# Kernel tuning notes

Measured on AMD Instinct MI355X. Metric: run time of the kernel, lower is better.

The kernel has to match this reference:

```python
import jax, jax.numpy as jnp
import numpy as np

DIM = 320
HEADS = 8
GROUPS = 32
KV_DIM = 768


def group_norm(x, scale, bias, groups=GROUPS, eps=1e-6):
    b, c, h, w = x.shape
    xg = x.reshape(b, groups, c // groups, h, w)
    mu = xg.mean(axis=(2, 3, 4), keepdims=True)
    var = xg.var(axis=(2, 3, 4), keepdims=True)
    xg = (xg - mu) * jax.lax.rsqrt(var + eps)
    x = xg.reshape(b, c, h, w)
    return x * scale[None, :, None, None] + bias[None, :, None, None]


def layer_norm(x, scale, bias, eps=1e-5):
    mu = x.mean(-1, keepdims=True)
    var = x.var(-1, keepdims=True)
    return (x - mu) * jax.lax.rsqrt(var + eps) * scale + bias


def cross_attention(x, kv, wq, wk, wv, wo, bo, heads=HEADS):
    # weights stored as [in, out] (transposed vs torch Linear)
    b, lq, d = x.shape
    lk = kv.shape[1]
    dh = d // heads
    q = (x @ wq).reshape(b, lq, heads, dh).transpose(0, 2, 1, 3)
    k = (kv @ wk).reshape(b, lk, heads, dh).transpose(0, 2, 1, 3)
    v = (kv @ wv).reshape(b, lk, heads, dh).transpose(0, 2, 1, 3)
    scores = jnp.einsum('bhqd,bhkd->bhqk', q, k) * (dh ** -0.5)
    attn = jax.nn.softmax(scores, axis=-1)
    out = jnp.einsum('bhqk,bhkd->bhqd', attn, v)
    out = out.transpose(0, 2, 1, 3).reshape(b, lq, d)
    return out @ wo + bo


def setup_inputs() -> dict:
    key = jax.random.key(0)
    ks = jax.random.split(key, 24)
    d = DIM
    s = 0.02
    inp = {
        'q': jax.random.normal(ks[0], (2, d, 64, 64), jnp.float32),
        'kv': jax.random.normal(ks[1], (2, 77, KV_DIM), jnp.float32),
        'gn_s': jnp.ones((d,), jnp.float32),
        'gn_b': jnp.zeros((d,), jnp.float32),
        'cin_w': jax.random.normal(ks[2], (d, d), jnp.float32) * s,
        'cin_b': jnp.zeros((d,), jnp.float32),
        'ln0_s': jnp.ones((d,), jnp.float32),
        'ln0_b': jnp.zeros((d,), jnp.float32),
        'a1_wq': jax.random.normal(ks[3], (d, d), jnp.float32) * s,
        'a1_wk': jax.random.normal(ks[4], (d, d), jnp.float32) * s,
        'a1_wv': jax.random.normal(ks[5], (d, d), jnp.float32) * s,
        'a1_wo': jax.random.normal(ks[6], (d, d), jnp.float32) * s,
        'a1_bo': jnp.zeros((d,), jnp.float32),
        'ln1_s': jnp.ones((d,), jnp.float32),
        'ln1_b': jnp.zeros((d,), jnp.float32),
        'a2_wq': jax.random.normal(ks[7], (d, d), jnp.float32) * s,
        'a2_wk': jax.random.normal(ks[8], (KV_DIM, d), jnp.float32) * s,
        'a2_wv': jax.random.normal(ks[9], (KV_DIM, d), jnp.float32) * s,
        'a2_wo': jax.random.normal(ks[10], (d, d), jnp.float32) * s,
        'a2_bo': jnp.zeros((d,), jnp.float32),
        'lnA_s': jnp.ones((d,), jnp.float32),
        'lnA_b': jnp.zeros((d,), jnp.float32),
        'fc0_w': jax.random.normal(ks[11], (d, 8 * d), jnp.float32) * s,
        'fc0_b': jnp.zeros((8 * d,), jnp.float32),
        'fc1_w': jax.random.normal(ks[12], (4 * d, d), jnp.float32) * s,
        'fc1_b': jnp.zeros((d,), jnp.float32),
        'cout_w': jax.random.normal(ks[13], (d, d), jnp.float32) * s,
        'cout_b': jnp.zeros((d,), jnp.float32),
    }
    return inp


def reference(q, kv, gn_s, gn_b, cin_w, cin_b, ln0_s, ln0_b,
              a1_wq, a1_wk, a1_wv, a1_wo, a1_bo, ln1_s, ln1_b,
              a2_wq, a2_wk, a2_wv, a2_wo, a2_bo, lnA_s, lnA_b,
              fc0_w, fc0_b, fc1_w, fc1_b, cout_w, cout_b):
    b, c, h, w = q.shape
    res1 = q
    x = group_norm(q, gn_s, gn_b)
    # 1x1 conv == channel matmul
    x = jnp.einsum('bchw,co->bohw', x, cin_w) + cin_b[None, :, None, None]
    x = x.transpose(0, 2, 3, 1).reshape(b, h * w, c)
    xn = layer_norm(x, ln0_s, ln0_b)
    x = cross_attention(xn, xn, a1_wq, a1_wk, a1_wv, a1_wo, a1_bo) + x
    x = cross_attention(layer_norm(x, ln1_s, ln1_b), kv,
                        a2_wq, a2_wk, a2_wv, a2_wo, a2_bo) + x
    res2 = x
    g = layer_norm(x, lnA_s, lnA_b) @ fc0_w + fc0_b
    half = g.shape[-1] // 2
    # GEGLU: value * GELU(gate); torch nn.GELU default is exact (erf)
    g = g[..., :half] * jax.nn.gelu(g[..., half:], approximate=False)
    x = g @ fc1_w + fc1_b + res2
    x = x.reshape(b, h, w, c).transpose(0, 3, 1, 2)
    x = jnp.einsum('bchw,co->bohw', x, cout_w) + cout_b[None, :, None, None] + res1
    return x
```

## Files before the change

### kernel.cpp

```cpp
#include <hip/hip_runtime.h>
#include <math.h>

typedef short short8 __attribute__((ext_vector_type(8)));
typedef float floatx4 __attribute__((ext_vector_type(4)));
typedef unsigned short ushort_t;
typedef unsigned int uint_t;

constexpr int BATCH   = 2;
constexpr int DIM     = 320;
constexpr int NHEADS  = 8;
constexpr int DH      = 40;
constexpr int NGROUPS = 32;
constexpr int CPG     = 10;
constexpr int SPATIAL = 4096;
constexpr int ROWS    = BATCH * SPATIAL;
constexpr int KVL     = 77;
constexpr int KVD     = 768;
constexpr int FF      = 1280;
constexpr int TQ      = 128;

#define QK_EXP2_SCALE 0.2281259062f

__device__ __forceinline__ ushort_t f2bf(float f) {
    uint_t u = __float_as_uint(f);
    u += 0x7FFFu + ((u >> 16) & 1u);
    return (ushort_t)(u >> 16);
}

__device__ __forceinline__ void gld16(const ushort_t* g, ushort_t* l) {
    __builtin_amdgcn_global_load_lds(
        (const __attribute__((address_space(1))) void*)g,
        (__attribute__((address_space(3))) void*)l, 16, 0, 0);
}

__global__ void zero_stats_kernel(float* stats) {
    if (threadIdx.x < 128) stats[threadIdx.x] = 0.f;
}

__global__ __launch_bounds__(256) void gn_partial_kernel(const float* __restrict__ q,
                                                         float* __restrict__ stats) {
    int slice = blockIdx.x, bg = blockIdx.y;
    const float* base = q + (size_t)bg * (CPG * SPATIAL) + slice * 2560;
    float s = 0.f, ss = 0.f;
#pragma unroll
    for (int j = 0; j < 10; j++) {
        float v = base[j * 256 + threadIdx.x];
        s += v; ss += v * v;
    }
    __shared__ float rs[256], rss[256];
    rs[threadIdx.x] = s; rss[threadIdx.x] = ss;
    __syncthreads();
    for (int off = 128; off > 0; off >>= 1) {
        if (threadIdx.x < off) {
            rs[threadIdx.x]  += rs[threadIdx.x + off];
            rss[threadIdx.x] += rss[threadIdx.x + off];
        }
        __syncthreads();
    }
    if (threadIdx.x == 0) {
        atomicAdd(&stats[bg * 2],     rs[0]);
        atomicAdd(&stats[bg * 2 + 1], rss[0]);
    }
}

__global__ void gn_apply_transpose_kernel(const float* __restrict__ q,
                                          const float* __restrict__ stats,
                                          const float* __restrict__ gs,
                                          const float* __restrict__ gb,
                                          ushort_t* __restrict__ out) {
    __shared__ float tile[32][33];
    int l0 = blockIdx.x * 32, c0 = blockIdx.y * 32, b = blockIdx.z;
    int tx = threadIdx.x, ty = threadIdx.y;
    int c = c0 + ty;
    int g = c / CPG;
    float s  = stats[(b * NGROUPS + g) * 2];
    float ss = stats[(b * NGROUPS + g) * 2 + 1];
    const float invn = 1.f / 40960.f;
    float mean = s * invn;
    float rstd = rsqrtf(ss * invn - mean * mean + 1e-6f);
    float v = q[((size_t)(b * DIM + c)) * SPATIAL + l0 + tx];
    tile[ty][tx] = (v - mean) * rstd * gs[c] + gb[c];
    __syncthreads();
    out[((size_t)(b * SPATIAL + l0 + ty)) * DIM + c0 + tx] = f2bf(tile[tx][ty]);
}

__global__ void out_transpose_kernel(const float* __restrict__ xin,
                                     const float* __restrict__ q,
                                     float* __restrict__ out) {
    __shared__ float tile[32][33];
    int l0 = blockIdx.x * 32, c0 = blockIdx.y * 32, b = blockIdx.z;
    int tx = threadIdx.x, ty = threadIdx.y;
    tile[ty][tx] = xin[((size_t)(b * SPATIAL + l0 + ty)) * DIM + c0 + tx];
    __syncthreads();
    size_t oi = ((size_t)(b * DIM + c0 + ty)) * SPATIAL + l0 + tx;
    out[oi] = tile[tx][ty] + q[oi];
}

__global__ __launch_bounds__(64) void ln_kernel(const float* __restrict__ x,
                                                const float* __restrict__ sc,
                                                const float* __restrict__ bi,
                                                ushort_t* __restrict__ out) {
    int row = blockIdx.x;
    const float* xr = x + (size_t)row * DIM;
    float v[5];
    float sum = 0.f, sq = 0.f;
#pragma unroll
    for (int j = 0; j < 5; j++) {
        v[j] = xr[threadIdx.x + j * 64];
        sum += v[j]; sq += v[j] * v[j];
    }
#pragma unroll
    for (int off = 32; off > 0; off >>= 1) {
        sum += __shfl_down(sum, off);
        sq  += __shfl_down(sq, off);
    }
    sum = __shfl(sum, 0); sq = __shfl(sq, 0);
    float mean = sum / (float)DIM;
    float rstd = rsqrtf(sq / (float)DIM - mean * mean + 1e-5f);
#pragma unroll
    for (int j = 0; j < 5; j++) {
        int i = threadIdx.x + j * 64;
        out[(size_t)row * DIM + i] = f2bf((v[j] - mean) * rstd * sc[i] + bi[i]);
    }
}

struct WSeg { const float* src; ushort_t* dst; int K; int N; int t0; };
struct WTab { WSeg s[12]; };

__global__ __launch_bounds__(256) void wtrans_all_kernel(WTab tab) {
    __shared__ float tile[32][33];
    int bid = blockIdx.x;
    int si = 0;
#pragma unroll
    for (int i = 1; i < 12; i++) if (bid >= tab.s[i].t0) si = i;
    WSeg sg = tab.s[si];
    int local = bid - sg.t0;
    int ntn = sg.N >> 5;
    int kt = local / ntn, nt = local - kt * ntn;
    int n0 = nt * 32, k0 = kt * 32;
    int tx = threadIdx.x & 31, ty8 = threadIdx.x >> 5;
    for (int r = ty8; r < 32; r += 8)
        tile[r][tx] = sg.src[(size_t)(k0 + r) * sg.N + n0 + tx];
    __syncthreads();
    for (int r = ty8; r < 32; r += 8)
        sg.dst[(size_t)(n0 + r) * sg.K + k0 + tx] = f2bf(tile[tx][r]);
}

__global__ void cvt_bf16_kernel(const float* __restrict__ src, ushort_t* __restrict__ dst, int n) {
    int i = blockIdx.x * 256 + threadIdx.x;
    if (i < n) dst[i] = f2bf(src[i]);
}

__global__ __launch_bounds__(256) void gemm128_kernel(
    const ushort_t* __restrict__ A, const ushort_t* __restrict__ Wt,
    const float* __restrict__ bias, const float* __restrict__ resid,
    float* __restrict__ Cf, ushort_t* __restrict__ Cb,
    int M, int N, int K, float qsc, int ncut)
{
    __shared__ __align__(16) ushort_t As[128][64];
    __shared__ __align__(16) ushort_t Bs[64][64];
    int tid = threadIdx.x;
    int wave = tid >> 6, lane = tid & 63;
    int l15 = tid & 15, quad = lane >> 4;
    int m0 = blockIdx.x * 128, n0 = blockIdx.y * 64;
    int lrow = lane >> 3, slot = lane & 7;
    floatx4 acc[2][4] = {};

    for (int k0 = 0; k0 < K; k0 += 64) {
#pragma unroll
        for (int t = 0; t < 4; t++) {
            int task = wave * 4 + t;
            int r = task * 8 + lrow;
            int gc = slot ^ (r & 7);
            gld16(&A[(size_t)(m0 + r) * K + k0 + gc * 8], &As[task * 8][0]);
        }
#pragma unroll
        for (int t = 0; t < 2; t++) {
            int task = wave * 2 + t;
            int r = task * 8 + lrow;
            int gc = slot ^ (r & 7);
            gld16(&Wt[(size_t)(n0 + r) * K + k0 + gc * 8], &Bs[task * 8][0]);
        }
        __syncthreads();
        short8 a[2][2], b[4][2];
#pragma unroll
        for (int g = 0; g < 2; g++) {
            int r = 32 * wave + 16 * g + l15;
            a[g][0] = *(const short8*)&As[r][(quad ^ (r & 7)) * 8];
            a[g][1] = *(const short8*)&As[r][((4 + quad) ^ (r & 7)) * 8];
        }
#pragma unroll
        for (int t = 0; t < 4; t++) {
            int r = 16 * t + l15;
            b[t][0] = *(const short8*)&Bs[r][(quad ^ (r & 7)) * 8];
            b[t][1] = *(const short8*)&Bs[r][((4 + quad) ^ (r & 7)) * 8];
        }
#pragma unroll
        for (int g = 0; g < 2; g++)
#pragma unroll
            for (int t = 0; t < 4; t++) {
                acc[g][t] = __builtin_amdgcn_mfma_f32_16x16x32_bf16(a[g][0], b[t][0], acc[g][t], 0, 0, 0);
                acc[g][t] = __builtin_amdgcn_mfma_f32_16x16x32_bf16(a[g][1], b[t][1], acc[g][t], 0, 0, 0);
            }
        __syncthreads();
    }

#pragma unroll
    for (int g = 0; g < 2; g++) {
        int mrow = m0 + 32 * wave + 16 * g + quad * 4;
#pragma unroll
        for (int t = 0; t < 4; t++) {
            int n = n0 + 16 * t + l15;
            float bv = bias ? bias[n] : 0.f;
            float sc = (n < ncut) ? qsc : 1.f;
#pragma unroll
            for (int i = 0; i < 4; i++) {
                int m = mrow + i;
                float v = acc[g][t][i] + bv;
                if (resid) v += resid[(size_t)m * N + n];
                v *= sc;
                if (Cf) Cf[(size_t)m * N + n] = v;
                if (Cb) Cb[(size_t)m * N + n] = f2bf(v);
            }
        }
    }
}

__global__ __launch_bounds__(256) void geglu128_kernel(
    const ushort_t* __restrict__ A, const ushort_t* __restrict__ Wt,
    const float* __restrict__ bias, ushort_t* __restrict__ C, int M)
{
    constexpr int K = 320;
    __shared__ __align__(16) ushort_t As[128][64];
    __shared__ __align__(16) ushort_t Bv[64][64];
    __shared__ __align__(16) ushort_t Bg[64][64];
    int tid = threadIdx.x;
    int wave = tid >> 6, lane = tid & 63;
    int l15 = tid & 15, quad = lane >> 4;
    int m0 = blockIdx.x * 128, n0 = blockIdx.y * 64;
    int lrow = lane >> 3, slot = lane & 7;
    floatx4 av[2][4] = {}, ag[2][4] = {};

    for (int k0 = 0; k0 < K; k0 += 64) {
#pragma unroll
        for (int t = 0; t < 4; t++) {
            int task = wave * 4 + t;
            int r = task * 8 + lrow;
            int gc = slot ^ (r & 7);
            gld16(&A[(size_t)(m0 + r) * K + k0 + gc * 8], &As[task * 8][0]);
        }
#pragma unroll
        for (int t = 0; t < 2; t++) {
            int task = wave * 2 + t;
            int r = task * 8 + lrow;
            int gc = slot ^ (r & 7);
            gld16(&Wt[(size_t)(n0 + r) * K + k0 + gc * 8],        &Bv[task * 8][0]);
            gld16(&Wt[(size_t)(FF + n0 + r) * K + k0 + gc * 8],   &Bg[task * 8][0]);
        }
        __syncthreads();
        short8 a[2][2], bv[4][2], bg[4][2];
#pragma unroll
        for (int g = 0; g < 2; g++) {
            int r = 32 * wave + 16 * g + l15;
            a[g][0] = *(const short8*)&As[r][(quad ^ (r & 7)) * 8];
            a[g][1] = *(const short8*)&As[r][((4 + quad) ^ (r & 7)) * 8];
        }
#pragma unroll
        for (int t = 0; t < 4; t++) {
            int r = 16 * t + l15;
            bv[t][0] = *(const short8*)&Bv[r][(quad ^ (r & 7)) * 8];
            bv[t][1] = *(const short8*)&Bv[r][((4 + quad) ^ (r & 7)) * 8];
            bg[t][0] = *(const short8*)&Bg[r][(quad ^ (r & 7)) * 8];
            bg[t][1] = *(const short8*)&Bg[r][((4 + quad) ^ (r & 7)) * 8];
        }
#pragma unroll
        for (int g = 0; g < 2; g++)
#pragma unroll
            for (int t = 0; t < 4; t++) {
                av[g][t] = __builtin_amdgcn_mfma_f32_16x16x32_bf16(a[g][0], bv[t][0], av[g][t], 0, 0, 0);
                av[g][t] = __builtin_amdgcn_mfma_f32_16x16x32_bf16(a[g][1], bv[t][1], av[g][t], 0, 0, 0);
                ag[g][t] = __builtin_amdgcn_mfma_f32_16x16x32_bf16(a[g][0], bg[t][0], ag[g][t], 0, 0, 0);
                ag[g][t] = __builtin_amdgcn_mfma_f32_16x16x32_bf16(a[g][1], bg[t][1], ag[g][t], 0, 0, 0);
            }
        __syncthreads();
    }

#pragma unroll
    for (int g = 0; g < 2; g++) {
        int mrow = m0 + 32 * wave + 16 * g + quad * 4;
#pragma unroll
        for (int t = 0; t < 4; t++) {
            int n = n0 + 16 * t + l15;
            float bb = bias[n], bgte = bias[FF + n];
#pragma unroll
            for (int i = 0; i < 4; i++) {
                float val  = av[g][t][i] + bb;
                float gate = ag[g][t][i] + bgte;
                float gl = 0.5f * gate * (1.f + erff(gate * 0.70710678118654752f));
                C[(size_t)(mrow + i) * FF + n] = f2bf(val * gl);
            }
        }
    }
}

__global__ __launch_bounds__(256) void gemm_small_kernel(
    const ushort_t* __restrict__ A, const ushort_t* __restrict__ Wt,
    ushort_t* __restrict__ Cb, int M, int N, int K)
{
    __shared__ __align__(16) ushort_t As[64][72];
    __shared__ __align__(16) ushort_t Bs[64][72];
    int tid = threadIdx.x;
    int wave = tid >> 6, l15 = tid & 15, quad = (tid & 63) >> 4;
    int m0 = blockIdx.x * 64, n0 = blockIdx.y * 64;
    floatx4 acc[4] = {};

    for (int k0 = 0; k0 < K; k0 += 64) {
#pragma unroll
        for (int p = 0; p < 2; p++) {
            int lin = p * 256 + tid;
            int r = lin >> 3, c8 = (lin & 7) * 8;
            int m = m0 + r;
            short8 avv = {};
            if (m < M) avv = *(const short8*)&A[(size_t)m * K + k0 + c8];
            *(short8*)&As[r][c8] = avv;
            *(short8*)&Bs[r][c8] = *(const short8*)&Wt[(size_t)(n0 + r) * K + k0 + c8];
        }
        __syncthreads();
        short8 a0 = *(const short8*)&As[16 * wave + l15][quad * 8];
        short8 a1 = *(const short8*)&As[16 * wave + l15][32 + quad * 8];
#pragma unroll
        for (int t = 0; t < 4; t++) {
            short8 b0 = *(const short8*)&Bs[16 * t + l15][quad * 8];
            short8 b1 = *(const short8*)&Bs[16 * t + l15][32 + quad * 8];
            acc[t] = __builtin_amdgcn_mfma_f32_16x16x32_bf16(a0, b0, acc[t], 0, 0, 0);
            acc[t] = __builtin_amdgcn_mfma_f32_16x16x32_bf16(a1, b1, acc[t], 0, 0, 0);
        }
        __syncthreads();
    }
    int mrow = m0 + 16 * wave + quad * 4;
#pragma unroll
    for (int t = 0; t < 4; t++) {
        int n = n0 + 16 * t + l15;
#pragma unroll
        for (int i = 0; i < 4; i++) {
            int m = mrow + i;
            if (m < M) Cb[(size_t)m * N + n] = f2bf(acc[t][i]);
        }
    }
}

template <int NPARTS>
__global__ __launch_bounds__(256) void flash_kernel(
    const ushort_t* __restrict__ Qg, const ushort_t* __restrict__ Kg,
    const ushort_t* __restrict__ Vg, ushort_t* __restrict__ Og,
    float* __restrict__ Opart, float* __restrict__ Lpart,
    int sQ, int sKV, int nk)
{
    __shared__ __align__(16) ushort_t QPs[8][130][8];
    __shared__ __align__(16) ushort_t Ks[8][64][8];
    __shared__ __align__(16) ushort_t VsT[48][72];

    int tid = threadIdx.x;
    int wave = tid >> 6, lane = tid & 63;
    int l15 = tid & 15, quad = lane >> 4;
    int qt = blockIdx.x, h = blockIdx.y;
    int b, kp;
    if (NPARTS == 2) { b = blockIdx.z >> 1; kp = blockIdx.z & 1; }
    else             { b = blockIdx.z;      kp = 0; }
    int q0 = qt * TQ;

    const ushort_t* Qb = Qg + (size_t)(b * SPATIAL + q0) * sQ + h * DH;
    const ushort_t* Kb = Kg + (size_t)b * nk * sKV + h * DH;
    const ushort_t* Vb = Vg + (size_t)b * nk * sKV + h * DH;

    const short8 z8 = {};
    for (int i = tid; i < 3 * 64; i += 256)
        *(short8*)&Ks[5 + (i >> 6)][i & 63][0] = z8;
    for (int i = tid; i < 8 * 72; i += 256)
        VsT[40 + i / 72][i % 72] = 0;
    if (tid < 72) VsT[40][tid] = 0x3F80;

    for (int t5 = wave; t5 < 10; t5 += 4) {
        int cid = t5 >> 1, half = t5 & 1;
        gld16(&Qb[(size_t)(half * 64 + lane) * sQ + cid * 8], &QPs[cid][half * 64][0]);
    }
    __syncthreads();

    short8 aq[2][2];
#pragma unroll
    for (int g = 0; g < 2; g++) {
        int r = 32 * wave + 16 * g + l15;
        aq[g][0] = *(const short8*)&QPs[quad][r][0];
        aq[g][1] = *(const short8*)&QPs[4 + quad][r][0];
    }

    floatx4 o[2][3] = {};

    int ntiles_all = (nk + 63) >> 6;
    int t_lo = (NPARTS == 2) ? kp * (ntiles_all >> 1) : 0;
    int t_hi = (NPARTS == 2) ? t_lo + (ntiles_all >> 1) : ntiles_all;

    for (int t = t_lo; t < t_hi; t++) {
        int k0 = t * 64;
        __syncthreads();
        for (int c = wave; c < 5; c += 4)
            gld16(&Kb[(size_t)(k0 + lane) * sKV + c * 8], &Ks[c][0][0]);
        for (int tk = tid; tk < 320; tk += 256) {
            int row = tk & 63, cid = tk >> 6;
            int kr = k0 + row;
            short8 v8 = z8;
            if (kr < nk) v8 = *(const short8*)&Vb[(size_t)kr * sKV + cid * 8];
#pragma unroll
            for (int j = 0; j < 8; j++) VsT[cid * 8 + j][row] = v8[j];
        }
        __syncthreads();

        floatx4 s[2][4] = {};
#pragma unroll
        for (int tt = 0; tt < 4; tt++) {
            short8 b0 = *(const short8*)&Ks[quad][16 * tt + l15][0];
            short8 b1 = *(const short8*)&Ks[4 + quad][16 * tt + l15][0];
#pragma unroll
            for (int g = 0; g < 2; g++) {
                s[g][tt] = __builtin_amdgcn_mfma_f32_16x16x32_bf16(aq[g][0], b0, s[g][tt], 0, 0, 0);
                s[g][tt] = __builtin_amdgcn_mfma_f32_16x16x32_bf16(aq[g][1], b1, s[g][tt], 0, 0, 0);
            }
        }

        bool full = (k0 + 64 <= nk);
#pragma unroll
        for (int g = 0; g < 2; g++) {
#pragma unroll
            for (int i = 0; i < 4; i++) {
                int row = 32 * wave + 16 * g + 4 * quad + i;
#pragma unroll
                for (int tt = 0; tt < 4; tt++) {
                    float x = s[g][tt][i];
                    if (!full && (k0 + 16 * tt + l15 >= nk)) x = -1e30f;
                    float pf = exp2f(x);
                    QPs[2 * tt + (l15 >> 3)][row][l15 & 7] =
                        (ushort_t)(__float_as_uint(pf) >> 16);
                }
            }
        }

        short8 vb[3][2];
#pragma unroll
        for (int t2 = 0; t2 < 3; t2++) {
            vb[t2][0] = *(const short8*)&VsT[16 * t2 + l15][quad * 8];
            vb[t2][1] = *(const short8*)&VsT[16 * t2 + l15][32 + quad * 8];
        }
#pragma unroll
        for (int g = 0; g < 2; g++) {
            int r = 32 * wave + 16 * g + l15;
            short8 p0 = *(const short8*)&QPs[quad][r][0];
            short8 p1 = *(const short8*)&QPs[4 + quad][r][0];
#pragma unroll
            for (int t2 = 0; t2 < 3; t2++) {
                o[g][t2] = __builtin_amdgcn_mfma_f32_16x16x32_bf16(p0, vb[t2][0], o[g][t2], 0, 0, 0);
                o[g][t2] = __builtin_amdgcn_mfma_f32_16x16x32_bf16(p1, vb[t2][1], o[g][t2], 0, 0, 0);
            }
        }
    }

    if (NPARTS == 1) {
        float inv[2][4];
#pragma unroll
        for (int g = 0; g < 2; g++)
#pragma unroll
            for (int i = 0; i < 4; i++)
                inv[g][i] = 1.f / __shfl(o[g][2][i], (lane & 48) | 8, 64);
#pragma unroll
        for (int g = 0; g < 2; g++)
#pragma unroll
            for (int t2 = 0; t2 < 3; t2++) {
                int c = 16 * t2 + l15;
                if (c < DH) {
#pragma unroll
                    for (int i = 0; i < 4; i++) {
                        size_t row = (size_t)(b * SPATIAL + q0 + 32 * wave + 16 * g + 4 * quad + i);
                        Og[row * DIM + h * DH + c] = f2bf(o[g][t2][i] * inv[g][i]);
                    }
                }
            }
    } else {
#pragma unroll
        for (int g = 0; g < 2; g++) {
#pragma unroll
            for (int t2 = 0; t2 < 3; t2++) {
                int c = 16 * t2 + l15;
                if (c < DH) {
#pragma unroll
                    for (int i = 0; i < 4; i++) {
                        size_t row = (size_t)(b * SPATIAL + q0 + 32 * wave + 16 * g + 4 * quad + i);
                        Opart[((size_t)kp * ROWS + row) * DIM + h * DH + c] = o[g][t2][i];
                    }
                }
            }
            if (l15 == 8) {
#pragma unroll
                for (int i = 0; i < 4; i++) {
                    size_t row = (size_t)(b * SPATIAL + q0 + 32 * wave + 16 * g + 4 * quad + i);
                    Lpart[((size_t)kp * ROWS + row) * NHEADS + h] = o[g][2][i];
                }
            }
        }
    }
}

__global__ __launch_bounds__(320) void attn_merge_kernel(
    const float* __restrict__ Op, const float* __restrict__ Lp,
    ushort_t* __restrict__ Og)
{
    int row = blockIdx.x, c = threadIdx.x;
    int h = c / DH;
    float l = Lp[(size_t)row * NHEADS + h] + Lp[((size_t)ROWS + row) * NHEADS + h];
    float o = Op[(size_t)row * DIM + c] + Op[((size_t)ROWS + row) * DIM + c];
    Og[(size_t)row * DIM + c] = f2bf(o / l);
}

extern "C" void kernel_launch(void* const* d_in, const int* in_sizes, int n_in,
                              void* d_out, int out_size, void* d_ws, size_t ws_size,
                              hipStream_t stream) {
    (void)in_sizes; (void)n_in; (void)out_size; (void)ws_size;
    const float* q      = (const float*)d_in[0];
    const float* kv     = (const float*)d_in[1];
    const float* gn_s   = (const float*)d_in[2];
    const float* gn_b   = (const float*)d_in[3];
    const float* cin_w  = (const float*)d_in[4];
    const float* cin_b  = (const float*)d_in[5];
    const float* ln0_s  = (const float*)d_in[6];
    const float* ln0_b  = (const float*)d_in[7];
    const float* a1_wq  = (const float*)d_in[8];
    const float* a1_wk  = (const float*)d_in[9];
    const float* a1_wv  = (const float*)d_in[10];
    const float* a1_wo  = (const float*)d_in[11];
    const float* a1_bo  = (const float*)d_in[12];
    const float* ln1_s  = (const float*)d_in[13];
    const float* ln1_b  = (const float*)d_in[14];
    const float* a2_wq  = (const float*)d_in[15];
    const float* a2_wk  = (const float*)d_in[16];
    const float* a2_wv  = (const float*)d_in[17];
    const float* a2_wo  = (const float*)d_in[18];
    const float* a2_bo  = (const float*)d_in[19];
    const float* lnA_s  = (const float*)d_in[20];
    const float* lnA_b  = (const float*)d_in[21];
    const float* fc0_w  = (const float*)d_in[22];
    const float* fc0_b  = (const float*)d_in[23];
    const float* fc1_w  = (const float*)d_in[24];
    const float* fc1_b  = (const float*)d_in[25];
    const float* cout_w = (const float*)d_in[26];
    const float* cout_b = (const float*)d_in[27];
    float* out = (float*)d_out;

    char* p = (char*)d_ws;
    auto carve = [&](size_t bytes) -> char* {
        char* r = p;
        p += (bytes + 255) & ~(size_t)255;
        return r;
    };
    float*    stats  = (float*)carve(512);
    float*    B0     = (float*)carve((size_t)ROWS * DIM * 4);
    float*    B2     = (float*)carve((size_t)ROWS * DIM * 4);
    ushort_t* gnO    = (ushort_t*)carve((size_t)ROWS * DIM * 2);
    ushort_t* ln0O   = (ushort_t*)carve((size_t)ROWS * DIM * 2);
    ushort_t* QKV    = (ushort_t*)carve((size_t)ROWS * 960 * 2);
    ushort_t* attnO  = (ushort_t*)carve((size_t)ROWS * DIM * 2);
    ushort_t* ln1O   = (ushort_t*)carve((size_t)ROWS * DIM * 2);
    ushort_t* Q2     = (ushort_t*)carve((size_t)ROWS * DIM * 2);
    ushort_t* KVc    = (ushort_t*)carve((size_t)BATCH * KVL * 640 * 2);
    ushort_t* lnAO   = (ushort_t*)carve((size_t)ROWS * DIM * 2);
    ushort_t* GLU    = (ushort_t*)carve((size_t)ROWS * FF * 2);
    ushort_t* X2     = (ushort_t*)carve((size_t)ROWS * DIM * 2);
    ushort_t* kvbf   = (ushort_t*)carve((size_t)BATCH * KVL * KVD * 2);
    ushort_t* qkv_t  = (ushort_t*)carve((size_t)960 * 320 * 2);
    ushort_t* cin_t  = (ushort_t*)carve((size_t)320 * 320 * 2);
    ushort_t* a1wo_t = (ushort_t*)carve((size_t)320 * 320 * 2);
    ushort_t* a2wq_t = (ushort_t*)carve((size_t)320 * 320 * 2);
    ushort_t* kvx_t  = (ushort_t*)carve((size_t)640 * 768 * 2);
    ushort_t* a2wo_t = (ushort_t*)carve((size_t)320 * 320 * 2);
    ushort_t* fc0_t  = (ushort_t*)carve((size_t)2560 * 320 * 2);
    ushort_t* fc1_t  = (ushort_t*)carve((size_t)320 * 1280 * 2);
    ushort_t* cout_t = (ushort_t*)carve((size_t)320 * 320 * 2);
    float* Opart = (float*)GLU;
    float* Lpart = (float*)gnO;

    auto gemm = [&](const ushort_t* A, const ushort_t* Wt, const float* bias,
                    const float* resid, float* Cf, ushort_t* Cb,
                    int M, int N, int K, float qsc = 1.f, int ncut = 0) {
        gemm128_kernel<<<dim3(M / 128, N / 64), 256, 0, stream>>>(
            A, Wt, bias, resid, Cf, Cb, M, N, K, qsc, ncut);
    };

    {
        WTab tab;
        int t0 = 0;
        auto seg = [&](int i, const float* s, ushort_t* d, int K, int N) {
            tab.s[i] = {s, d, K, N, t0};
            t0 += (K / 32) * (N / 32);
        };
        seg(0,  cin_w,  cin_t,             320, 320);
        seg(1,  a1_wq,  qkv_t,             320, 320);
        seg(2,  a1_wk,  qkv_t + 320 * 320, 320, 320);
        seg(3,  a1_wv,  qkv_t + 640 * 320, 320, 320);
        seg(4,  a1_wo,  a1wo_t,            320, 320);
        seg(5,  a2_wq,  a2wq_t,            320, 320);
        seg(6,  a2_wk,  kvx_t,             768, 320);
        seg(7,  a2_wv,  kvx_t + 320 * 768, 768, 320);
        seg(8,  a2_wo,  a2wo_t,            320, 320);
        seg(9,  fc0_w,  fc0_t,             320, 2560);
        seg(10, fc1_w,  fc1_t,             1280, 320);
        seg(11, cout_w, cout_t,            320, 320);
        wtrans_all_kernel<<<t0, 256, 0, stream>>>(tab);
    }
    {
        int n = BATCH * KVL * KVD;
        cvt_bf16_kernel<<<(n + 255) / 256, 256, 0, stream>>>(kv, kvbf, n);
    }

    zero_stats_kernel<<<1, 128, 0, stream>>>(stats);
    gn_partial_kernel<<<dim3(16, 64), 256, 0, stream>>>(q, stats);
    gn_apply_transpose_kernel<<<dim3(SPATIAL / 32, DIM / 32, BATCH), dim3(32, 32), 0, stream>>>(
        q, stats, gn_s, gn_b, gnO);
    gemm(gnO, cin_t, cin_b, nullptr, B0, nullptr, ROWS, DIM, DIM);

    ln_kernel<<<ROWS, 64, 0, stream>>>(B0, ln0_s, ln0_b, ln0O);
    gemm(ln0O, qkv_t, nullptr, nullptr, nullptr, QKV, ROWS, 960, DIM, QK_EXP2_SCALE, 320);
    flash_kernel<2><<<dim3(SPATIAL / TQ, NHEADS, BATCH * 2), 256, 0, stream>>>(
        QKV, QKV + 320, QKV + 640, nullptr, Opart, Lpart, 960, 960, SPATIAL);
    attn_merge_kernel<<<ROWS, 320, 0, stream>>>(Opart, Lpart, attnO);
    gemm(attnO, a1wo_t, a1_bo, B0, B0, nullptr, ROWS, DIM, DIM);

    ln_kernel<<<ROWS, 64, 0, stream>>>(B0, ln1_s, ln1_b, ln1O);
    gemm(ln1O, a2wq_t, nullptr, nullptr, nullptr, Q2, ROWS, DIM, DIM, QK_EXP2_SCALE, 320);
    gemm_small_kernel<<<dim3(3, 10), 256, 0, stream>>>(kvbf, kvx_t, KVc, BATCH * KVL, 640, KVD);
    flash_kernel<1><<<dim3(SPATIAL / TQ, NHEADS, BATCH), 256, 0, stream>>>(
        Q2, KVc, KVc + 320, attnO, nullptr, nullptr, 320, 640, KVL);
    gemm(attnO, a2wo_t, a2_bo, B0, B0, nullptr, ROWS, DIM, DIM);

    ln_kernel<<<ROWS, 64, 0, stream>>>(B0, lnA_s, lnA_b, lnAO);
    geglu128_kernel<<<dim3(ROWS / 128, FF / 64), 256, 0, stream>>>(lnAO, fc0_t, fc0_b, GLU, ROWS);
    gemm(GLU, fc1_t, fc1_b, B0, nullptr, X2, ROWS, DIM, FF);

    gemm(X2, cout_t, cout_b, nullptr, B2, nullptr, ROWS, DIM, DIM);
    out_transpose_kernel<<<dim3(SPATIAL / 32, DIM / 32, BATCH), dim3(32, 32), 0, stream>>>(B2, q, out);
}
```

Baseline: 430.9 us.

## Fuse conv-out with transpose, pre-transpose V, merge small kernels, retile GEMMs

```diff
diff --git a/kernel.cpp b/kernel.cpp
--- a/kernel.cpp
+++ b/kernel.cpp
@@ -31,10 +31,6 @@
     __builtin_amdgcn_global_load_lds(
         (const __attribute__((address_space(1))) void*)g,
         (__attribute__((address_space(3))) void*)l, 16, 0, 0);
-}
-
-__global__ void zero_stats_kernel(float* stats) {
-    if (threadIdx.x < 128) stats[threadIdx.x] = 0.f;
 }
 
 __global__ __launch_bounds__(256) void gn_partial_kernel(const float* __restrict__ q,
@@ -84,29 +80,18 @@
     out[((size_t)(b * SPATIAL + l0 + ty)) * DIM + c0 + tx] = f2bf(tile[tx][ty]);
 }
 
-__global__ void out_transpose_kernel(const float* __restrict__ xin,
-                                     const float* __restrict__ q,
-                                     float* __restrict__ out) {
-    __shared__ float tile[32][33];
-    int l0 = blockIdx.x * 32, c0 = blockIdx.y * 32, b = blockIdx.z;
-    int tx = threadIdx.x, ty = threadIdx.y;
-    tile[ty][tx] = xin[((size_t)(b * SPATIAL + l0 + ty)) * DIM + c0 + tx];
-    __syncthreads();
-    size_t oi = ((size_t)(b * DIM + c0 + ty)) * SPATIAL + l0 + tx;
-    out[oi] = tile[tx][ty] + q[oi];
-}
-
-__global__ __launch_bounds__(64) void ln_kernel(const float* __restrict__ x,
-                                                const float* __restrict__ sc,
-                                                const float* __restrict__ bi,
-                                                ushort_t* __restrict__ out) {
-    int row = blockIdx.x;
+__global__ __launch_bounds__(256) void ln_kernel(const float* __restrict__ x,
+                                                 const float* __restrict__ sc,
+                                                 const float* __restrict__ bi,
+                                                 ushort_t* __restrict__ out) {
+    int row = blockIdx.x * 4 + (threadIdx.x >> 6);
+    int lane = threadIdx.x & 63;
     const float* xr = x + (size_t)row * DIM;
     float v[5];
     float sum = 0.f, sq = 0.f;
 #pragma unroll
     for (int j = 0; j < 5; j++) {
-        v[j] = xr[threadIdx.x + j * 64];
+        v[j] = xr[lane + j * 64];
         sum += v[j]; sq += v[j] * v[j];
     }
 #pragma unroll
@@ -119,17 +104,32 @@
     float rstd = rsqrtf(sq / (float)DIM - mean * mean + 1e-5f);
 #pragma unroll
     for (int j = 0; j < 5; j++) {
-        int i = threadIdx.x + j * 64;
+        int i = lane + j * 64;
         out[(size_t)row * DIM + i] = f2bf((v[j] - mean) * rstd * sc[i] + bi[i]);
     }
 }
 
 struct WSeg { const float* src; ushort_t* dst; int K; int N; int t0; };
-struct WTab { WSeg s[12]; };
+struct WTab {
+    WSeg s[12];
+    const float* cvt_src; ushort_t* cvt_dst; int cvt_n; int cvt_t0;
+    float* stats;
+};
 
 __global__ __launch_bounds__(256) void wtrans_all_kernel(WTab tab) {
+    int bid = blockIdx.x;
+    if (bid >= tab.cvt_t0) {
+        int local = bid - tab.cvt_t0;
+        int base = local * 8192;
+#pragma unroll
+        for (int j = 0; j < 32; j++) {
+            int i = base + j * 256 + threadIdx.x;
+            if (i < tab.cvt_n) tab.cvt_dst[i] = f2bf(tab.cvt_src[i]);
+        }
+        if (local == 0 && threadIdx.x < 128) tab.stats[threadIdx.x] = 0.f;
+        return;
+    }
     __shared__ float tile[32][33];
-    int bid = blockIdx.x;
     int si = 0;
 #pragma unroll
     for (int i = 1; i < 12; i++) if (bid >= tab.s[i].t0) si = i;
@@ -146,30 +146,52 @@
         sg.dst[(size_t)(n0 + r) * sg.K + k0 + tx] = f2bf(tile[tx][r]);
 }
 
-__global__ void cvt_bf16_kernel(const float* __restrict__ src, ushort_t* __restrict__ dst, int n) {
-    int i = blockIdx.x * 256 + threadIdx.x;
-    if (i < n) dst[i] = f2bf(src[i]);
-}
-
-__global__ __launch_bounds__(256) void gemm128_kernel(
+__global__ __launch_bounds__(256) void vtrans_kernel(const ushort_t* __restrict__ src,
+                                                     ushort_t* __restrict__ dst,
+                                                     int stride, int headOff,
+                                                     int L, int Lpad) {
+    __shared__ ushort_t tile[32][41];
+    int bh = blockIdx.y, b = bh >> 3, h = bh & 7;
+    int l0 = blockIdx.x * 32;
+    for (int idx = threadIdx.x; idx < 32 * 40; idx += 256) {
+        int l = idx / 40, d = idx - l * 40;
+        ushort_t v = 0;
+        if (l0 + l < L)
+            v = src[(size_t)(b * L + l0 + l) * stride + headOff + h * DH + d];
+        tile[l][d] = v;
+    }
+    __syncthreads();
+    for (int idx = threadIdx.x; idx < 48 * 32; idx += 256) {
+        int d = idx >> 5, li = idx & 31;
+        ushort_t v;
+        if (d < 40)      v = tile[li][d];
+        else if (d == 40) v = 0x3F80;
+        else             v = 0;
+        dst[((size_t)bh * 48 + d) * Lpad + l0 + li] = v;
+    }
+}
+
+template <int TM>
+__global__ __launch_bounds__(256) void gemm_bf16_kernel(
     const ushort_t* __restrict__ A, const ushort_t* __restrict__ Wt,
     const float* __restrict__ bias, const float* __restrict__ resid,
     float* __restrict__ Cf, ushort_t* __restrict__ Cb,
     int M, int N, int K, float qsc, int ncut)
 {
-    __shared__ __align__(16) ushort_t As[128][64];
+    constexpr int G = TM / 64;
+    __shared__ __align__(16) ushort_t As[TM][64];
     __shared__ __align__(16) ushort_t Bs[64][64];
     int tid = threadIdx.x;
     int wave = tid >> 6, lane = tid & 63;
     int l15 = tid & 15, quad = lane >> 4;
-    int m0 = blockIdx.x * 128, n0 = blockIdx.y * 64;
+    int m0 = blockIdx.x * TM, n0 = blockIdx.y * 64;
     int lrow = lane >> 3, slot = lane & 7;
-    floatx4 acc[2][4] = {};
+    floatx4 acc[G][4] = {};
 
     for (int k0 = 0; k0 < K; k0 += 64) {
 #pragma unroll
-        for (int t = 0; t < 4; t++) {
-            int task = wave * 4 + t;
+        for (int t = 0; t < TM / 32; t++) {
+            int task = wave * (TM / 32) + t;
             int r = task * 8 + lrow;
             int gc = slot ^ (r & 7);
             gld16(&A[(size_t)(m0 + r) * K + k0 + gc * 8], &As[task * 8][0]);
@@ -182,10 +204,10 @@
             gld16(&Wt[(size_t)(n0 + r) * K + k0 + gc * 8], &Bs[task * 8][0]);
         }
         __syncthreads();
-        short8 a[2][2], b[4][2];
-#pragma unroll
-        for (int g = 0; g < 2; g++) {
-            int r = 32 * wave + 16 * g + l15;
+        short8 a[G][2], b[4][2];
+#pragma unroll
+        for (int g = 0; g < G; g++) {
+            int r = (TM / 4) * wave + 16 * g + l15;
             a[g][0] = *(const short8*)&As[r][(quad ^ (r & 7)) * 8];
             a[g][1] = *(const short8*)&As[r][((4 + quad) ^ (r & 7)) * 8];
         }
@@ -196,7 +218,7 @@
             b[t][1] = *(const short8*)&Bs[r][((4 + quad) ^ (r & 7)) * 8];
         }
 #pragma unroll
-        for (int g = 0; g < 2; g++)
+        for (int g = 0; g < G; g++)
 #pragma unroll
             for (int t = 0; t < 4; t++) {
                 acc[g][t] = __builtin_amdgcn_mfma_f32_16x16x32_bf16(a[g][0], b[t][0], acc[g][t], 0, 0, 0);
@@ -206,8 +228,8 @@
     }
 
 #pragma unroll
-    for (int g = 0; g < 2; g++) {
-        int mrow = m0 + 32 * wave + 16 * g + quad * 4;
+    for (int g = 0; g < G; g++) {
+        int mrow = m0 + (TM / 4) * wave + 16 * g + quad * 4;
 #pragma unroll
         for (int t = 0; t < 4; t++) {
             int n = n0 + 16 * t + l15;
@@ -254,8 +276,8 @@
             int task = wave * 2 + t;
             int r = task * 8 + lrow;
             int gc = slot ^ (r & 7);
-            gld16(&Wt[(size_t)(n0 + r) * K + k0 + gc * 8],        &Bv[task * 8][0]);
-            gld16(&Wt[(size_t)(FF + n0 + r) * K + k0 + gc * 8],   &Bg[task * 8][0]);
+            gld16(&Wt[(size_t)(n0 + r) * K + k0 + gc * 8],      &Bv[task * 8][0]);
+            gld16(&Wt[(size_t)(FF + n0 + r) * K + k0 + gc * 8], &Bg[task * 8][0]);
         }
         __syncthreads();
         short8 a[2][2], bv[4][2], bg[4][2];
@@ -299,6 +321,79 @@
                 float gl = 0.5f * gate * (1.f + erff(gate * 0.70710678118654752f));
                 C[(size_t)(mrow + i) * FF + n] = f2bf(val * gl);
             }
+        }
+    }
+}
+
+__global__ __launch_bounds__(256) void gemm_convout_kernel(
+    const ushort_t* __restrict__ A, const ushort_t* __restrict__ Wt,
+    const float* __restrict__ bias, const float* __restrict__ qres,
+    float* __restrict__ out)
+{
+    constexpr int K = 320, N = 320;
+    __shared__ __align__(16) ushort_t As[64][64];
+    __shared__ __align__(16) ushort_t Bs[64][64];
+    __shared__ float Cf[64][68];
+    int tid = threadIdx.x;
+    int wave = tid >> 6, lane = tid & 63;
+    int l15 = tid & 15, quad = lane >> 4;
+    int m0 = blockIdx.x * 64, n0 = blockIdx.y * 64;
+    int lrow = lane >> 3, slot = lane & 7;
+    floatx4 acc[4] = {};
+
+    for (int k0 = 0; k0 < K; k0 += 64) {
+#pragma unroll
+        for (int t = 0; t < 2; t++) {
+            int task = wave * 2 + t;
+            int r = task * 8 + lrow;
+            int gc = slot ^ (r & 7);
+            gld16(&A[(size_t)(m0 + r) * K + k0 + gc * 8], &As[task * 8][0]);
+            gld16(&Wt[(size_t)(n0 + r) * K + k0 + gc * 8], &Bs[task * 8][0]);
+        }
+        __syncthreads();
+        short8 a0, a1, b[4][2];
+        {
+            int r = 16 * wave + l15;
+            a0 = *(const short8*)&As[r][(quad ^ (r & 7)) * 8];
+            a1 = *(const short8*)&As[r][((4 + quad) ^ (r & 7)) * 8];
+        }
+#pragma unroll
+        for (int t = 0; t < 4; t++) {
+            int r = 16 * t + l15;
+            b[t][0] = *(const short8*)&Bs[r][(quad ^ (r & 7)) * 8];
+            b[t][1] = *(const short8*)&Bs[r][((4 + quad) ^ (r & 7)) * 8];
+        }
+#pragma unroll
+        for (int t = 0; t < 4; t++) {
+            acc[t] = __builtin_amdgcn_mfma_f32_16x16x32_bf16(a0, b[t][0], acc[t], 0, 0, 0);
+            acc[t] = __builtin_amdgcn_mfma_f32_16x16x32_bf16(a1, b[t][1], acc[t], 0, 0, 0);
+        }
+        __syncthreads();
+    }
+
+#pragma unroll
+    for (int t = 0; t < 4; t++) {
+        int n = 16 * t + l15;
+        float bv = bias[n0 + n];
+        int mbase = 16 * wave + 4 * quad;
+#pragma unroll
+        for (int i = 0; i < 4; i++)
+            Cf[n][mbase + i] = acc[t][i] + bv;
+    }
+    __syncthreads();
+    {
+        int n = tid >> 2, j = tid & 3;
+        int bq = m0 >> 12;
+        int l0 = m0 & 4095;
+        size_t goff = ((size_t)(bq * DIM + n0 + n)) * SPATIAL + l0 + j * 16;
+        const float4* qr = (const float4*)(qres + goff);
+        float4* op = (float4*)(out + goff);
+#pragma unroll
+        for (int c = 0; c < 4; c++) {
+            float4 v = *(const float4*)&Cf[n][j * 16 + c * 4];
+            float4 qv = qr[c];
+            v.x += qv.x; v.y += qv.y; v.z += qv.z; v.w += qv.w;
+            op[c] = v;
         }
     }
 }
@@ -352,13 +447,13 @@
 template <int NPARTS>
 __global__ __launch_bounds__(256) void flash_kernel(
     const ushort_t* __restrict__ Qg, const ushort_t* __restrict__ Kg,
-    const ushort_t* __restrict__ Vg, ushort_t* __restrict__ Og,
+    const ushort_t* __restrict__ VT, ushort_t* __restrict__ Og,
     float* __restrict__ Opart, float* __restrict__ Lpart,
-    int sQ, int sKV, int nk)
+    int sQ, int sKV, int Lpad, int nk)
 {
     __shared__ __align__(16) ushort_t QPs[8][130][8];
     __shared__ __align__(16) ushort_t Ks[8][64][8];
-    __shared__ __align__(16) ushort_t VsT[48][72];
+    __shared__ __align__(16) ushort_t VsT[48][64];
 
     int tid = threadIdx.x;
     int wave = tid >> 6, lane = tid & 63;
@@ -369,16 +464,15 @@
     else             { b = blockIdx.z;      kp = 0; }
     int q0 = qt * TQ;
 
-    const ushort_t* Qb = Qg + (size_t)(b * SPATIAL + q0) * sQ + h * DH;
-    const ushort_t* Kb = Kg + (size_t)b * nk * sKV + h * DH;
-    const ushort_t* Vb = Vg + (size_t)b * nk * sKV + h * DH;
+    const ushort_t* Qb  = Qg + (size_t)(b * SPATIAL + q0) * sQ + h * DH;
+    const ushort_t* Kb  = Kg + (size_t)b * nk * sKV + h * DH;
+    const ushort_t* VTb = VT + (size_t)(b * NHEADS + h) * 48 * Lpad;
 
     const short8 z8 = {};
     for (int i = tid; i < 3 * 64; i += 256)
         *(short8*)&Ks[5 + (i >> 6)][i & 63][0] = z8;
-    for (int i = tid; i < 8 * 72; i += 256)
-        VsT[40 + i / 72][i % 72] = 0;
-    if (tid < 72) VsT[40][tid] = 0x3F80;
+    for (int i = tid; i < 3 * 130; i += 256)
+        *(short8*)&QPs[5 + i / 130][i % 130][0] = z8;
 
     for (int t5 = wave; t5 < 10; t5 += 4) {
         int cid = t5 >> 1, half = t5 & 1;
@@ -405,13 +499,10 @@
         __syncthreads();
         for (int c = wave; c < 5; c += 4)
             gld16(&Kb[(size_t)(k0 + lane) * sKV + c * 8], &Ks[c][0][0]);
-        for (int tk = tid; tk < 320; tk += 256) {
-            int row = tk & 63, cid = tk >> 6;
-            int kr = k0 + row;
-            short8 v8 = z8;
-            if (kr < nk) v8 = *(const short8*)&Vb[(size_t)kr * sKV + cid * 8];
-#pragma unroll
-            for (int j = 0; j < 8; j++) VsT[cid * 8 + j][row] = v8[j];
+        for (int c = wave; c < 6; c += 4) {
+            int r8 = lane >> 3;
+            int gc = (lane & 7) ^ r8;
+            gld16(&VTb[(size_t)(c * 8 + r8) * Lpad + k0 + gc * 8], &VsT[c * 8][0]);
         }
         __syncthreads();
 
@@ -433,13 +524,14 @@
 #pragma unroll
             for (int i = 0; i < 4; i++) {
                 int row = 32 * wave + 16 * g + 4 * quad + i;
+                int rw = (4 * quad + i) & 7;
 #pragma unroll
                 for (int tt = 0; tt < 4; tt++) {
                     float x = s[g][tt][i];
                     if (!full && (k0 + 16 * tt + l15 >= nk)) x = -1e30f;
                     float pf = exp2f(x);
-                    QPs[2 * tt + (l15 >> 3)][row][l15 & 7] =
-                        (ushort_t)(__float_as_uint(pf) >> 16);
+                    int c = (2 * tt + (l15 >> 3)) ^ rw;
+                    QPs[c][row][l15 & 7] = (ushort_t)(__float_as_uint(pf) >> 16);
                 }
             }
         }
@@ -447,14 +539,16 @@
         short8 vb[3][2];
 #pragma unroll
         for (int t2 = 0; t2 < 3; t2++) {
-            vb[t2][0] = *(const short8*)&VsT[16 * t2 + l15][quad * 8];
-            vb[t2][1] = *(const short8*)&VsT[16 * t2 + l15][32 + quad * 8];
+            int R = 16 * t2 + l15;
+            vb[t2][0] = *(const short8*)&VsT[R][(quad ^ (l15 & 7)) * 8];
+            vb[t2][1] = *(const short8*)&VsT[R][((4 + quad) ^ (l15 & 7)) * 8];
         }
 #pragma unroll
         for (int g = 0; g < 2; g++) {
             int r = 32 * wave + 16 * g + l15;
-            short8 p0 = *(const short8*)&QPs[quad][r][0];
-            short8 p1 = *(const short8*)&QPs[4 + quad][r][0];
+            int rw = l15 & 7;
+            short8 p0 = *(const short8*)&QPs[quad ^ rw][r][0];
+            short8 p1 = *(const short8*)&QPs[(4 + quad) ^ rw][r][0];
 #pragma unroll
             for (int t2 = 0; t2 < 3; t2++) {
                 o[g][t2] = __builtin_amdgcn_mfma_f32_16x16x32_bf16(p0, vb[t2][0], o[g][t2], 0, 0, 0);
@@ -561,7 +655,6 @@
     };
     float*    stats  = (float*)carve(512);
     float*    B0     = (float*)carve((size_t)ROWS * DIM * 4);
-    float*    B2     = (float*)carve((size_t)ROWS * DIM * 4);
     ushort_t* gnO    = (ushort_t*)carve((size_t)ROWS * DIM * 2);
     ushort_t* ln0O   = (ushort_t*)carve((size_t)ROWS * DIM * 2);
     ushort_t* QKV    = (ushort_t*)carve((size_t)ROWS * 960 * 2);
@@ -573,6 +666,8 @@
     ushort_t* GLU    = (ushort_t*)carve((size_t)ROWS * FF * 2);
     ushort_t* X2     = (ushort_t*)carve((size_t)ROWS * DIM * 2);
     ushort_t* kvbf   = (ushort_t*)carve((size_t)BATCH * KVL * KVD * 2);
+    ushort_t* VTs    = (ushort_t*)carve((size_t)16 * 48 * SPATIAL * 2);
+    ushort_t* VTc    = (ushort_t*)carve((size_t)16 * 48 * 128 * 2);
     ushort_t* qkv_t  = (ushort_t*)carve((size_t)960 * 320 * 2);
     ushort_t* cin_t  = (ushort_t*)carve((size_t)320 * 320 * 2);
     ushort_t* a1wo_t = (ushort_t*)carve((size_t)320 * 320 * 2);
@@ -585,10 +680,16 @@
     float* Opart = (float*)GLU;
     float* Lpart = (float*)gnO;
 
-    auto gemm = [&](const ushort_t* A, const ushort_t* Wt, const float* bias,
-                    const float* resid, float* Cf, ushort_t* Cb,
-                    int M, int N, int K, float qsc = 1.f, int ncut = 0) {
-        gemm128_kernel<<<dim3(M / 128, N / 64), 256, 0, stream>>>(
+    auto gemm64 = [&](const ushort_t* A, const ushort_t* Wt, const float* bias,
+                      const float* resid, float* Cf, ushort_t* Cb,
+                      int M, int N, int K, float qsc = 1.f, int ncut = 0) {
+        gemm_bf16_kernel<64><<<dim3(M / 64, N / 64), 256, 0, stream>>>(
+            A, Wt, bias, resid, Cf, Cb, M, N, K, qsc, ncut);
+    };
+    auto gemm128 = [&](const ushort_t* A, const ushort_t* Wt, const float* bias,
+                       const float* resid, float* Cf, ushort_t* Cb,
+                       int M, int N, int K, float qsc = 1.f, int ncut = 0) {
+        gemm_bf16_kernel<128><<<dim3(M / 128, N / 64), 256, 0, stream>>>(
             A, Wt, bias, resid, Cf, Cb, M, N, K, qsc, ncut);
     };
 
@@ -611,37 +712,38 @@
         seg(9,  fc0_w,  fc0_t,             320, 2560);
         seg(10, fc1_w,  fc1_t,             1280, 320);
         seg(11, cout_w, cout_t,            320, 320);
-        wtrans_all_kernel<<<t0, 256, 0, stream>>>(tab);
-    }
-    {
-        int n = BATCH * KVL * KVD;
-        cvt_bf16_kernel<<<(n + 255) / 256, 256, 0, stream>>>(kv, kvbf, n);
-    }
-
-    zero_stats_kernel<<<1, 128, 0, stream>>>(stats);
+        tab.cvt_src = kv; tab.cvt_dst = kvbf;
+        tab.cvt_n = BATCH * KVL * KVD; tab.cvt_t0 = t0;
+        tab.stats = stats;
+        int ncvt_blk = (tab.cvt_n + 8191) / 8192;
+        wtrans_all_kernel<<<t0 + ncvt_blk, 256, 0, stream>>>(tab);
+    }
+
     gn_partial_kernel<<<dim3(16, 64), 256, 0, stream>>>(q, stats);
     gn_apply_transpose_kernel<<<dim3(SPATIAL / 32, DIM / 32, BATCH), dim3(32, 32), 0, stream>>>(
         q, stats, gn_s, gn_b, gnO);
-    gemm(gnO, cin_t, cin_b, nullptr, B0, nullptr, ROWS, DIM, DIM);
-
-    ln_kernel<<<ROWS, 64, 0, stream>>>(B0, ln0_s, ln0_b, ln0O);
-    gemm(ln0O, qkv_t, nullptr, nullptr, nullptr, QKV, ROWS, 960, DIM, QK_EXP2_SCALE, 320);
+    gemm64(gnO, cin_t, cin_b, nullptr, B0, nullptr, ROWS, DIM, DIM);
+
+    ln_kernel<<<ROWS / 4, 256, 0, stream>>>(B0, ln0_s, ln0_b, ln0O);
+    gemm128(ln0O, qkv_t, nullptr, nullptr, nullptr, QKV, ROWS, 960, DIM, QK_EXP2_SCALE, 320);
+    vtrans_kernel<<<dim3(SPATIAL / 32, 16), 256, 0, stream>>>(QKV, VTs, 960, 640, SPATIAL, SPATIAL);
     flash_kernel<2><<<dim3(SPATIAL / TQ, NHEADS, BATCH * 2), 256, 0, stream>>>(
-        QKV, QKV + 320, QKV + 640, nullptr, Opart, Lpart, 960, 960, SPATIAL);
+        QKV, QKV + 320, VTs, nullptr, Opart, Lpart, 960, 960, SPATIAL, SPATIAL);
     attn_merge_kernel<<<ROWS, 320, 0, stream>>>(Opart, Lpart, attnO);
-    gemm(attnO, a1wo_t, a1_bo, B0, B0, nullptr, ROWS, DIM, DIM);
-
-    ln_kernel<<<ROWS, 64, 0, stream>>>(B0, ln1_s, ln1_b, ln1O);
-    gemm(ln1O, a2wq_t, nullptr, nullptr, nullptr, Q2, ROWS, DIM, DIM, QK_EXP2_SCALE, 320);
+    gemm64(attnO, a1wo_t, a1_bo, B0, B0, nullptr, ROWS, DIM, DIM);
+
+    ln_kernel<<<ROWS / 4, 256, 0, stream>>>(B0, ln1_s, ln1_b, ln1O);
+    gemm64(ln1O, a2wq_t, nullptr, nullptr, nullptr, Q2, ROWS, DIM, DIM, QK_EXP2_SCALE, 320);
     gemm_small_kernel<<<dim3(3, 10), 256, 0, stream>>>(kvbf, kvx_t, KVc, BATCH * KVL, 640, KVD);
+    vtrans_kernel<<<dim3(4, 16), 256, 0, stream>>>(KVc, VTc, 640, 320, KVL, 128);
     flash_kernel<1><<<dim3(SPATIAL / TQ, NHEADS, BATCH), 256, 0, stream>>>(
-        Q2, KVc, KVc + 320, attnO, nullptr, nullptr, 320, 640, KVL);
-    gemm(attnO, a2wo_t, a2_bo, B0, B0, nullptr, ROWS, DIM, DIM);
-
-    ln_kernel<<<ROWS, 64, 0, stream>>>(B0, lnA_s, lnA_b, lnAO);
+        Q2, KVc, VTc, attnO, nullptr, nullptr, 320, 640, 128, KVL);
+    gemm64(attnO, a2wo_t, a2_bo, B0, B0, nullptr, ROWS, DIM, DIM);
+
+    ln_kernel<<<ROWS / 4, 256, 0, stream>>>(B0, lnA_s, lnA_b, lnAO);
     geglu128_kernel<<<dim3(ROWS / 128, FF / 64), 256, 0, stream>>>(lnAO, fc0_t, fc0_b, GLU, ROWS);
-    gemm(GLU, fc1_t, fc1_b, B0, nullptr, X2, ROWS, DIM, FF);
-
-    gemm(X2, cout_t, cout_b, nullptr, B2, nullptr, ROWS, DIM, DIM);
-    out_transpose_kernel<<<dim3(SPATIAL / 32, DIM / 32, BATCH), dim3(32, 32), 0, stream>>>(B2, q, out);
-}
+    gemm64(GLU, fc1_t, fc1_b, B0, nullptr, X2, ROWS, DIM, FF);
+
+    gemm_convout_kernel<<<dim3(ROWS / 64, DIM / 64), 256, 0, stream>>>(
+        X2, cout_t, cout_b, q, out);
+}
```

Result: no change. 437.2 us (+1.5%).
